# Optimization experiments

Hardware: AMD Instinct MI355X
Metric: run time of the kernel (lower is better)

The kernel has to match this reference:

```python
import jax, jax.numpy as jnp
import numpy as np

R = 8          # number of areas of interest (regions)
C = 32         # n_channels_per_region
NPR = 128      # neurons per region (contiguous layout)
RKEEP = 6      # R - int(R * r_ratio), r_ratio = 0.25
HID = 1024     # hidden_size
NLAT = 160     # sum of n_lat over regions (20 * 8)


def setup_inputs() -> dict:
    key = jax.random.key(0)
    ks = jax.random.split(key, 8)
    B, T = 32, 1024
    N = R * NPR
    spikes = jax.random.normal(ks[0], (B, T, N), jnp.float32)
    # per-(session,area) Linear weights, stacked over regions: [R, C, NPR]
    W_area = jax.random.normal(ks[1], (R, C, NPR), jnp.float32) / np.sqrt(NPR)
    b_area = jax.random.normal(ks[2], (R, C), jnp.float32) * 0.01
    U_W = jax.random.normal(ks[3], (HID, R * C), jnp.float32) / np.sqrt(R * C)
    U_b = jnp.zeros((HID,), jnp.float32)
    V_W = jax.random.normal(ks[4], (NLAT, HID), jnp.float32) / np.sqrt(HID)
    V_b = jnp.zeros((NLAT,), jnp.float32)
    # per-sample random region permutation (MAE-style mask): argsort of noise
    noise = jax.random.uniform(ks[5], (B, R))
    ids_shuffle = jnp.argsort(noise, axis=1).astype(jnp.int32)
    return dict(spikes=spikes, W_area=W_area, b_area=b_area,
                U_W=U_W, U_b=U_b, V_W=V_W, V_b=V_b, ids_shuffle=ids_shuffle)


def reference(spikes, W_area, b_area, U_W, U_b, V_W, V_b, ids_shuffle):
    B, T, N = spikes.shape
    # Stitcher: per-area gather -> small Linear -> scatter into region slots.
    # Regions are contiguous (neuron n belongs to region n // NPR), so the
    # torch.where gather is a static reshape; preprocess_X is identity
    # (smoothing=False, halfbin_X=0).
    x = spikes.reshape(B, T, R, NPR)
    region_emb = jnp.einsum('btrn,rcn->btrc', x, W_area) + b_area  # [B,T,R,C]
    # random_mask over regions: keep RKEEP regions per sample
    ids_keep = ids_shuffle[:, :RKEEP]                 # [B, RKEEP]
    ids_restore = jnp.argsort(ids_shuffle, axis=1)    # [B, R]
    x_masked = jnp.take_along_axis(region_emb, ids_keep[:, None, :, None], axis=2)
    # append zero mask tokens and restore original region order
    mask_tok = jnp.zeros((B, T, R - RKEEP, C), region_emb.dtype)
    x_full = jnp.concatenate([x_masked, mask_tok], axis=2)        # [B,T,R,C]
    x_rest = jnp.take_along_axis(x_full, ids_restore[:, None, :, None], axis=2)
    h = x_rest.reshape(B, T, R * C)
    u = h @ U_W.T + U_b                                # [B,T,HID]
    return u @ V_W.T + V_b                             # [B,T,NLAT]
```

## Files before the change

### kernel.cpp

```cpp
#include <hip/hip_runtime.h>
#include <hip/hip_bf16.h>


typedef float f32x4 __attribute__((ext_vector_type(4)));
typedef __bf16 bf16x8 __attribute__((ext_vector_type(8)));

#define KSPLIT 16

__global__ __launch_bounds__(256) void pa_kernel(const float* __restrict__ V_W,
                                                 const float* __restrict__ U_W,
                                                 float* __restrict__ M_part) {
    const int rc = threadIdx.x;
    const int lq = blockIdx.x >> 4;
    const int ck = blockIdx.x & 15;
    const int l0 = lq * 4;
    const int h0 = ck * 64;
    float a0 = 0.f, a1 = 0.f, a2 = 0.f, a3 = 0.f;
#pragma unroll 8
    for (int hh = 0; hh < 64; ++hh) {
        const int h = h0 + hh;
        const float u = U_W[h * 256 + rc];
        a0 += V_W[(l0 + 0) * 1024 + h] * u;
        a1 += V_W[(l0 + 1) * 1024 + h] * u;
        a2 += V_W[(l0 + 2) * 1024 + h] * u;
        a3 += V_W[(l0 + 3) * 1024 + h] * u;
    }
    float* dst = M_part + (size_t)ck * 160 * 256;
    dst[(l0 + 0) * 256 + rc] = a0;
    dst[(l0 + 1) * 256 + rc] = a1;
    dst[(l0 + 2) * 256 + rc] = a2;
    dst[(l0 + 3) * 256 + rc] = a3;
}

__global__ __launch_bounds__(256) void pb_kernel(const float* __restrict__ M_part,
                                                 const float* __restrict__ W_area,
                                                 const float* __restrict__ b_area,
                                                 const float* __restrict__ V_W,
                                                 const float* __restrict__ U_b,
                                                 const float* __restrict__ V_b,
                                                 __bf16* __restrict__ F,
                                                 float* __restrict__ bias_area,
                                                 float* __restrict__ bias0) {
    const int l = blockIdx.x >> 2;
    const int p4 = blockIdx.x & 3;
    const int tid = threadIdx.x;
    __shared__ float Mrow[256];
    __shared__ float red[256];

    float m = 0.f;
#pragma unroll
    for (int p = 0; p < KSPLIT; ++p) m += M_part[(size_t)(p * 160 + l) * 256 + tid];
    Mrow[tid] = m;

    float p0 = 0.f;
#pragma unroll
    for (int hh = 0; hh < 4; ++hh) {
        const int h = tid + hh * 256;
        p0 += V_W[(size_t)l * 1024 + h] * U_b[h];
    }
    red[tid] = p0;
    __syncthreads();

    {
        const int rn = p4 * 256 + tid;
        const int r = rn >> 7, n = rn & 127;
        float acc = 0.f;
#pragma unroll
        for (int c = 0; c < 32; ++c)
            acc += Mrow[r * 32 + c] * W_area[((r * 32 + c) << 7) + n];
        F[(size_t)l * 1024 + rn] = (__bf16)acc;
    }

    if (p4 == 0) {
        if (tid < 8) {
            const int r = tid;
            float acc = 0.f;
            for (int c = 0; c < 32; ++c) acc += Mrow[r * 32 + c] * b_area[r * 32 + c];
            bias_area[l * 8 + r] = acc;
        }
        for (int off = 128; off > 0; off >>= 1) {
            __syncthreads();
            if (tid < off) red[tid] += red[tid + off];
        }
        if (tid == 0) bias0[l] = V_b[l] + red[0];
    }
}

__global__ __launch_bounds__(256, 4) void main_kernel(const float* __restrict__ spikes,
                                                      const int* __restrict__ ids,
                                                      const __bf16* __restrict__ F,
                                                      const float* __restrict__ bias_area,
                                                      const float* __restrict__ bias0,
                                                      float* __restrict__ out) {
    const int tid = threadIdx.x;
    const int lane = tid & 63;
    const int wave = tid >> 6;
    const int s = lane & 15;
    const int q = lane >> 4;
    const int half = wave & 1;
    const int tt = blockIdx.x * 2 + (wave >> 1);
    const int tok0 = tt * 16;
    const int b = tok0 >> 10;

    int rj[6];
#pragma unroll
    for (int j = 0; j < 6; ++j) rj[j] = ids[b * 8 + j];

    f32x4 acc[5];
#pragma unroll
    for (int nt = 0; nt < 5; ++nt) acc[nt] = (f32x4){0.f, 0.f, 0.f, 0.f};

    const __bf16* Fh = F + (size_t)(half * 80 + s) * 1024;

#pragma unroll 1
    for (int j = 0; j < 6; ++j) {
        const int colbase = rj[j] * 128;
        float4 rawA[4][2];
        {
            const float* rowp = spikes + (size_t)(tok0 + s) * 1024 + colbase + q * 8;
#pragma unroll
            for (int kk = 0; kk < 4; ++kk) {
                rawA[kk][0] = *(const float4*)(rowp + kk * 32);
                rawA[kk][1] = *(const float4*)(rowp + kk * 32 + 4);
            }
        }
#pragma unroll
        for (int kk = 0; kk < 4; ++kk) {
            const int col = colbase + kk * 32 + q * 8;
            bf16x8 bf[5];
#pragma unroll
            for (int nt = 0; nt < 5; ++nt)
                bf[nt] = *(const bf16x8*)(Fh + (size_t)nt * 16 * 1024 + col);
            const float4 lo = rawA[kk][0];
            const float4 hi = rawA[kk][1];
            bf16x8 af;
            af[0] = (__bf16)lo.x; af[1] = (__bf16)lo.y;
            af[2] = (__bf16)lo.z; af[3] = (__bf16)lo.w;
            af[4] = (__bf16)hi.x; af[5] = (__bf16)hi.y;
            af[6] = (__bf16)hi.z; af[7] = (__bf16)hi.w;
#pragma unroll
            for (int nt = 0; nt < 5; ++nt)
                acc[nt] = __builtin_amdgcn_mfma_f32_16x16x32_bf16(
                    af, bf[nt], acc[nt], 0, 0, 0);
        }
    }

#pragma unroll
    for (int nt = 0; nt < 5; ++nt) {
        const int l = half * 80 + nt * 16 + s;
        float bias = bias0[l];
#pragma unroll
        for (int j = 0; j < 6; ++j) bias += bias_area[l * 8 + rj[j]];
        const int tk = tok0 + q * 4;
#pragma unroll
        for (int i = 0; i < 4; ++i)
            out[(size_t)(tk + i) * 160 + l] = acc[nt][i] + bias;
    }
}

extern "C" void kernel_launch(void* const* d_in, const int* in_sizes, int n_in,
                              void* d_out, int out_size, void* d_ws, size_t ws_size,
                              hipStream_t stream) {
    (void)in_sizes; (void)n_in; (void)out_size; (void)ws_size;
    const float* spikes = (const float*)d_in[0];
    const float* W_area = (const float*)d_in[1];
    const float* b_area = (const float*)d_in[2];
    const float* U_W    = (const float*)d_in[3];
    const float* U_b    = (const float*)d_in[4];
    const float* V_W    = (const float*)d_in[5];
    const float* V_b    = (const float*)d_in[6];
    const int*   ids    = (const int*)d_in[7];
    float* out = (float*)d_out;

    char* ws = (char*)d_ws;
    float*  M_part    = (float*)ws;
    __bf16* F         = (__bf16*)(ws + 2621440);
    float*  bias_area = (float*)(ws + 2949120);
    float*  bias0     = (float*)(ws + 2954240);

    pa_kernel<<<640, 256, 0, stream>>>(V_W, U_W, M_part);
    pb_kernel<<<640, 256, 0, stream>>>(M_part, W_area, b_area, V_W, U_b, V_b,
                                       F, bias_area, bias0);
    main_kernel<<<1024, 256, 0, stream>>>(spikes, ids, F, bias_area, bias0, out);
}
```

Baseline: 274.8 us.

## Double-buffer spike tiles into LDS and pack F for coalesced MFMA loads

The main kernel now stages each wave's spike rows for the next kept region into LDS with async global_load_lds while it computes the current region. Each wave covers all 160 outputs (10 accumulators) for its 16 tokens, using 128-thread blocks. F is written by pb_kernel in a packed layout so each lane's B-fragment loads are contiguous. This aims to hide global-load latency and improve coalescing, at the cost of more registers per wave and lower occupancy.

```diff
diff --git a/kernel.cpp b/kernel.cpp
--- a/kernel.cpp
+++ b/kernel.cpp
@@ -38,7 +38,7 @@
                                                  const float* __restrict__ V_W,
                                                  const float* __restrict__ U_b,
                                                  const float* __restrict__ V_b,
-                                                 __bf16* __restrict__ F,
+                                                 __bf16* __restrict__ F_packed,
                                                  float* __restrict__ bias_area,
                                                  float* __restrict__ bias0) {
     const int l = blockIdx.x >> 2;
@@ -68,7 +68,10 @@
 #pragma unroll
         for (int c = 0; c < 32; ++c)
             acc += Mrow[r * 32 + c] * W_area[((r * 32 + c) << 7) + n];
-        F[(size_t)l * 1024 + rn] = (__bf16)acc;
+        const int kk = n >> 5, q = (n >> 3) & 3, i = n & 7;
+        const int nt = l >> 4, s = l & 15;
+        const size_t idx = ((size_t)(r * 4 + kk) * 10 + nt) * 512 + (q * 16 + s) * 8 + i;
+        F_packed[idx] = (__bf16)acc;
     }
 
     if (p4 == 0) {
@@ -86,9 +89,9 @@
     }
 }
 
-__global__ __launch_bounds__(256, 4) void main_kernel(const float* __restrict__ spikes,
+__global__ __launch_bounds__(128, 2) void main_kernel(const float* __restrict__ spikes,
                                                       const int* __restrict__ ids,
-                                                      const __bf16* __restrict__ F,
+                                                      const __bf16* __restrict__ Fp,
                                                       const float* __restrict__ bias_area,
                                                       const float* __restrict__ bias0,
                                                       float* __restrict__ out) {
@@ -97,61 +100,69 @@
     const int wave = tid >> 6;
     const int s = lane & 15;
     const int q = lane >> 4;
-    const int half = wave & 1;
-    const int tt = blockIdx.x * 2 + (wave >> 1);
-    const int tok0 = tt * 16;
-    const int b = tok0 >> 10;
+    const int tokw = blockIdx.x * 32 + wave * 16;
+    const int b = blockIdx.x >> 5;
+
+    __shared__ float tile[2][2][2048];
 
     int rj[6];
 #pragma unroll
     for (int j = 0; j < 6; ++j) rj[j] = ids[b * 8 + j];
 
-    f32x4 acc[5];
+    f32x4 acc[10];
 #pragma unroll
-    for (int nt = 0; nt < 5; ++nt) acc[nt] = (f32x4){0.f, 0.f, 0.f, 0.f};
+    for (int nt = 0; nt < 10; ++nt) acc[nt] = (f32x4){0.f, 0.f, 0.f, 0.f};
 
-    const __bf16* Fh = F + (size_t)(half * 80 + s) * 1024;
+    const int r2 = lane >> 5;
+    const int c32 = lane & 31;
+
+    auto stage = [&](int buf, int reg) {
+        const float* src = spikes + (size_t)(tokw + r2) * 1024 + reg * 128 + c32 * 4;
+        float* ldsw = &tile[wave][buf][0];
+#pragma unroll
+        for (int i = 0; i < 8; ++i)
+            __builtin_amdgcn_global_load_lds(
+                (const __attribute__((address_space(1))) float*)(src + i * 2048),
+                (__attribute__((address_space(3))) float*)(ldsw + i * 256),
+                16, 0, 0);
+    };
+
+    stage(0, rj[0]);
 
 #pragma unroll 1
     for (int j = 0; j < 6; ++j) {
-        const int colbase = rj[j] * 128;
-        float4 rawA[4][2];
-        {
-            const float* rowp = spikes + (size_t)(tok0 + s) * 1024 + colbase + q * 8;
-#pragma unroll
-            for (int kk = 0; kk < 4; ++kk) {
-                rawA[kk][0] = *(const float4*)(rowp + kk * 32);
-                rawA[kk][1] = *(const float4*)(rowp + kk * 32 + 4);
-            }
-        }
+        if (j < 5) stage((j + 1) & 1, rj[j + 1]);
+        asm volatile("s_waitcnt vmcnt(8)" ::: "memory");
+
+        const float* arow = &tile[wave][j & 1][(s >> 1) * 256 + (s & 1) * 128];
 #pragma unroll
         for (int kk = 0; kk < 4; ++kk) {
-            const int col = colbase + kk * 32 + q * 8;
-            bf16x8 bf[5];
+            bf16x8 bfr[10];
+            const __bf16* fb = Fp + ((size_t)(rj[j] * 4 + kk) * 10) * 512 + lane * 8;
 #pragma unroll
-            for (int nt = 0; nt < 5; ++nt)
-                bf[nt] = *(const bf16x8*)(Fh + (size_t)nt * 16 * 1024 + col);
-            const float4 lo = rawA[kk][0];
-            const float4 hi = rawA[kk][1];
+            for (int nt = 0; nt < 10; ++nt)
+                bfr[nt] = *(const bf16x8*)(fb + nt * 512);
+            const f32x4 a0 = *(const f32x4*)(arow + kk * 32 + q * 8);
+            const f32x4 a1 = *(const f32x4*)(arow + kk * 32 + q * 8 + 4);
             bf16x8 af;
-            af[0] = (__bf16)lo.x; af[1] = (__bf16)lo.y;
-            af[2] = (__bf16)lo.z; af[3] = (__bf16)lo.w;
-            af[4] = (__bf16)hi.x; af[5] = (__bf16)hi.y;
-            af[6] = (__bf16)hi.z; af[7] = (__bf16)hi.w;
+            af[0] = (__bf16)a0.x; af[1] = (__bf16)a0.y;
+            af[2] = (__bf16)a0.z; af[3] = (__bf16)a0.w;
+            af[4] = (__bf16)a1.x; af[5] = (__bf16)a1.y;
+            af[6] = (__bf16)a1.z; af[7] = (__bf16)a1.w;
 #pragma unroll
-            for (int nt = 0; nt < 5; ++nt)
+            for (int nt = 0; nt < 10; ++nt)
                 acc[nt] = __builtin_amdgcn_mfma_f32_16x16x32_bf16(
-                    af, bf[nt], acc[nt], 0, 0, 0);
+                    af, bfr[nt], acc[nt], 0, 0, 0);
         }
     }
 
 #pragma unroll
-    for (int nt = 0; nt < 5; ++nt) {
-        const int l = half * 80 + nt * 16 + s;
+    for (int nt = 0; nt < 10; ++nt) {
+        const int l = nt * 16 + s;
         float bias = bias0[l];
 #pragma unroll
         for (int j = 0; j < 6; ++j) bias += bias_area[l * 8 + rj[j]];
-        const int tk = tok0 + q * 4;
+        const int tk = tokw + q * 4;
 #pragma unroll
         for (int i = 0; i < 4; ++i)
             out[(size_t)(tk + i) * 160 + l] = acc[nt][i] + bias;
@@ -174,12 +185,12 @@
 
     char* ws = (char*)d_ws;
     float*  M_part    = (float*)ws;
-    __bf16* F         = (__bf16*)(ws + 2621440);
+    __bf16* F_packed  = (__bf16*)(ws + 2621440);
     float*  bias_area = (float*)(ws + 2949120);
     float*  bias0     = (float*)(ws + 2954240);
 
     pa_kernel<<<640, 256, 0, stream>>>(V_W, U_W, M_part);
     pb_kernel<<<640, 256, 0, stream>>>(M_part, W_area, b_area, V_W, U_b, V_b,
-                                       F, bias_area, bias0);
-    main_kernel<<<1024, 256, 0, stream>>>(spikes, ids, F, bias_area, bias0, out);
+                                       F_packed, bias_area, bias0);
+    main_kernel<<<1024, 128, 0, stream>>>(spikes, ids, F_packed, bias_area, bias0, out);
 }
```

After: 236.4 us. 14.0% less time.
